# Kernel tuning notes

Measured on AMD Instinct MI355X. Metric: run time of the kernel, lower is better.

Reference implementation:

```python
import jax, jax.numpy as jnp
import numpy as np

BETA = 0.1
NUM_LAYERS = 2  # GT layers inside each FastGTN


def densify(edge_index, edge_weight, num_nodes):
    # edge_index: [T, 2, E] int, edge_weight: [T, E] -> dense [T, N, N]
    T, _, E = edge_index.shape
    t_ids = jnp.broadcast_to(jnp.arange(T)[:, None], (T, E))
    dense = jnp.zeros((T, num_nodes, num_nodes), dtype=edge_weight.dtype)
    return dense.at[t_ids, edge_index[:, 0, :], edge_index[:, 1, :]].add(edge_weight)


def fast_gtn(dense_A, X, Ws, conv_w, lin_w, lin_b, num_nodes):
    # Ws: [C, w_in, w_out]; conv_w: [L, C, T]; lin_w: [C*w_out, w_out]
    H = jnp.einsum('nk,ckh->cnh', X, Ws)              # [C, N, w_out]
    X_ = jax.lax.stop_gradient(H)                      # clone().detach()
    for l in range(NUM_LAYERS):
        filt = jax.nn.softmax(conv_w[l], axis=1)       # [C, T]
        adj = jnp.einsum('ct,tij->cij', filt, dense_A) # [C, N, N]
        H = jnp.einsum('cij,cjh->cih', adj, H)         # graph conv per channel
    H_ = jax.nn.relu(BETA * X_ + (1.0 - BETA) * H)     # [C, N, w_out]
    H_ = jnp.transpose(H_, (1, 0, 2)).reshape(num_nodes, -1)  # [N, C*w_out]
    return jax.nn.relu(H_ @ lin_w + lin_b)             # [N, w_out]


def setup_inputs() -> dict:
    key = jax.random.key(0)
    ks = jax.random.split(key, 12)
    T, E, N = 4, 131072, 4096
    C, F_IN, H_OUT = 2, 128, 64
    edge_index = jax.random.randint(ks[0], (T, 2, E), 0, N, dtype=jnp.int64)
    edge_weight = jax.random.uniform(ks[1], (T, E), dtype=jnp.float32)
    X = jax.random.normal(ks[2], (N, F_IN), dtype=jnp.float32)
    def glorot(k, shape):
        fan_in, fan_out = shape[-2], shape[-1]
        s = jnp.sqrt(6.0 / (fan_in + fan_out))
        return jax.random.uniform(k, shape, jnp.float32, -s, s)
    # FastGTN #1 (w_in=F_IN)
    Ws1 = glorot(ks[3], (C, F_IN, H_OUT))
    conv_w1 = 0.1 * jax.random.normal(ks[4], (NUM_LAYERS, C, T), dtype=jnp.float32)
    lin_w1 = glorot(ks[5], (C * H_OUT, H_OUT))
    lin_b1 = jnp.zeros((H_OUT,), jnp.float32)
    # FastGTN #2 (w_in=H_OUT)
    Ws2 = glorot(ks[6], (C, H_OUT, H_OUT))
    conv_w2 = 0.1 * jax.random.normal(ks[7], (NUM_LAYERS, C, T), dtype=jnp.float32)
    lin_w2 = glorot(ks[8], (C * H_OUT, H_OUT))
    lin_b2 = jnp.zeros((H_OUT,), jnp.float32)
    return {"edge_index": edge_index, "edge_weight": edge_weight, "X": X,
            "Ws1": Ws1, "conv_w1": conv_w1, "lin_w1": lin_w1, "lin_b1": lin_b1,
            "Ws2": Ws2, "conv_w2": conv_w2, "lin_w2": lin_w2, "lin_b2": lin_b2}


def reference(edge_index, edge_weight, X, Ws1, conv_w1, lin_w1, lin_b1,
              Ws2, conv_w2, lin_w2, lin_b2):
    N = X.shape[0]
    dense_A = densify(edge_index, edge_weight, N)      # [T, N, N]
    H = fast_gtn(dense_A, X, Ws1, conv_w1, lin_w1, lin_b1, N)
    H = fast_gtn(dense_A, H, Ws2, conv_w2, lin_w2, lin_b2, N)
    return H
```

## Files before the change

### kernel.cpp

```cpp
#include <hip/hip_runtime.h>

#define E_EDGES 131072
#define N_NODES 4096
#define HOUT    64
#define NE_TOT  (4 * E_EDGES)
#define CAP     256
#define CSTRIDE 16
#define SC_NBLK 64
#define SC_NTHR 1024
#define SC_EPB  (NE_TOT / SC_NBLK)
#define SC_EPT  (SC_EPB / SC_NTHR)

__device__ __forceinline__ unsigned short f2bf(float x) {
    unsigned u = __float_as_uint(x);
    return (unsigned short)((u + 0x7FFFu + ((u >> 16) & 1u)) >> 16);
}
__device__ __forceinline__ float bf2f(unsigned b) {
    return __uint_as_float(b << 16);
}

__device__ __forceinline__ void softmax4(const float* __restrict__ cw,
                                         int layer, int c, float f[4]) {
#pragma unroll
    for (int t = 0; t < 4; ++t) f[t] = cw[(layer * 2 + c) * 4 + t];
    float m = fmaxf(fmaxf(f[0], f[1]), fmaxf(f[2], f[3]));
    float s = 0.f;
#pragma unroll
    for (int t = 0; t < 4; ++t) { f[t] = expf(f[t] - m); s += f[t]; }
    float inv = 1.0f / s;
#pragma unroll
    for (int t = 0; t < 4; ++t) f[t] *= inv;
}

__device__ __forceinline__ float selw(const float f[4], int t) {
    float a = (t & 1) ? f[1] : f[0];
    float b = (t & 1) ? f[3] : f[2];
    return (t & 2) ? b : a;
}

__device__ __forceinline__ void fma8(float acc[8], float w, uint4 v) {
    acc[0] += w * bf2f(v.x & 0xFFFFu); acc[1] += w * bf2f(v.x >> 16);
    acc[2] += w * bf2f(v.y & 0xFFFFu); acc[3] += w * bf2f(v.y >> 16);
    acc[4] += w * bf2f(v.z & 0xFFFFu); acc[5] += w * bf2f(v.z >> 16);
    acc[6] += w * bf2f(v.w & 0xFFFFu); acc[7] += w * bf2f(v.w >> 16);
}

__device__ __forceinline__ uint4 pack8(const float acc[8]) {
    uint4 r;
    r.x = (unsigned)f2bf(acc[0]) | ((unsigned)f2bf(acc[1]) << 16);
    r.y = (unsigned)f2bf(acc[2]) | ((unsigned)f2bf(acc[3]) << 16);
    r.z = (unsigned)f2bf(acc[4]) | ((unsigned)f2bf(acc[5]) << 16);
    r.w = (unsigned)f2bf(acc[6]) | ((unsigned)f2bf(acc[7]) << 16);
    return r;
}

__device__ __forceinline__ void spmm_row2c(const unsigned* __restrict__ rowe, int len,
                                           const unsigned* __restrict__ H16,
                                           const float f0[4], const float f1[4],
                                           int lane, float a0[8], float a1[8]) {
    int g  = lane >> 3;
    int hq = lane & 7;
#pragma unroll
    for (int j = 0; j < 8; ++j) { a0[j] = 0.f; a1[j] = 0.f; }
    int e = 0;
    for (; e + 32 <= len; e += 32) {
        unsigned r0 = rowe[e + g];
        unsigned r1 = rowe[e + 8 + g];
        unsigned r2 = rowe[e + 16 + g];
        unsigned r3 = rowe[e + 24 + g];
        int   d0 = r0 & 0xFFF, t0 = (r0 >> 12) & 3;
        int   d1 = r1 & 0xFFF, t1 = (r1 >> 12) & 3;
        int   d2 = r2 & 0xFFF, t2 = (r2 >> 12) & 3;
        int   d3 = r3 & 0xFFF, t3 = (r3 >> 12) & 3;
        float w0 = bf2f(r0 >> 16), w1 = bf2f(r1 >> 16);
        float w2 = bf2f(r2 >> 16), w3 = bf2f(r3 >> 16);
        uint4 v00 = ((const uint4*)(H16 + (d0 * 2 + 0) * 32))[hq];
        uint4 v01 = ((const uint4*)(H16 + (d0 * 2 + 1) * 32))[hq];
        uint4 v10 = ((const uint4*)(H16 + (d1 * 2 + 0) * 32))[hq];
        uint4 v11 = ((const uint4*)(H16 + (d1 * 2 + 1) * 32))[hq];
        uint4 v20 = ((const uint4*)(H16 + (d2 * 2 + 0) * 32))[hq];
        uint4 v21 = ((const uint4*)(H16 + (d2 * 2 + 1) * 32))[hq];
        uint4 v30 = ((const uint4*)(H16 + (d3 * 2 + 0) * 32))[hq];
        uint4 v31 = ((const uint4*)(H16 + (d3 * 2 + 1) * 32))[hq];
        fma8(a0, w0 * selw(f0, t0), v00);
        fma8(a1, w0 * selw(f1, t0), v01);
        fma8(a0, w1 * selw(f0, t1), v10);
        fma8(a1, w1 * selw(f1, t1), v11);
        fma8(a0, w2 * selw(f0, t2), v20);
        fma8(a1, w2 * selw(f1, t2), v21);
        fma8(a0, w3 * selw(f0, t3), v30);
        fma8(a1, w3 * selw(f1, t3), v31);
    }
    for (; e + 8 <= len; e += 8) {
        unsigned r0 = rowe[e + g];
        int   d0 = r0 & 0xFFF, t0 = (r0 >> 12) & 3;
        float w0 = bf2f(r0 >> 16);
        uint4 v00 = ((const uint4*)(H16 + (d0 * 2 + 0) * 32))[hq];
        uint4 v01 = ((const uint4*)(H16 + (d0 * 2 + 1) * 32))[hq];
        fma8(a0, w0 * selw(f0, t0), v00);
        fma8(a1, w0 * selw(f1, t0), v01);
    }
    if (g < len - e) {
        unsigned r0 = rowe[e + g];
        int   d0 = r0 & 0xFFF, t0 = (r0 >> 12) & 3;
        float w0 = bf2f(r0 >> 16);
        uint4 v00 = ((const uint4*)(H16 + (d0 * 2 + 0) * 32))[hq];
        uint4 v01 = ((const uint4*)(H16 + (d0 * 2 + 1) * 32))[hq];
        fma8(a0, w0 * selw(f0, t0), v00);
        fma8(a1, w0 * selw(f1, t0), v01);
    }
#pragma unroll
    for (int j = 0; j < 8; ++j) {
        a0[j] += __shfl_xor(a0[j], 8);
        a0[j] += __shfl_xor(a0[j], 16);
        a0[j] += __shfl_xor(a0[j], 32);
        a1[j] += __shfl_xor(a1[j], 8);
        a1[j] += __shfl_xor(a1[j], 16);
        a1[j] += __shfl_xor(a1[j], 32);
    }
}

__global__ void __launch_bounds__(256)
zinit_kernel(const float* __restrict__ X, const float* __restrict__ Ws,
             float* __restrict__ H0, unsigned* __restrict__ H016,
             int* __restrict__ cursor) {
    int idx = blockIdx.x * 256 + threadIdx.x;
    if (idx < N_NODES * CSTRIDE) cursor[idx] = 0;
    int h = idx & 63;
    int n = (idx >> 6) & (N_NODES - 1);
    int c = idx >> 18;
    const float4* xv = (const float4*)(X + n * 128);
    const float*  w  = Ws + c * 128 * HOUT + h;
    float acc = 0.f;
#pragma unroll 8
    for (int k4 = 0; k4 < 32; ++k4) {
        float4 xx = xv[k4];
        acc += xx.x * w[(k4 * 4 + 0) * HOUT];
        acc += xx.y * w[(k4 * 4 + 1) * HOUT];
        acc += xx.z * w[(k4 * 4 + 2) * HOUT];
        acc += xx.w * w[(k4 * 4 + 3) * HOUT];
    }
    H0[idx] = acc;
    ((unsigned short*)H016)[(n * 2 + c) * HOUT + h] = f2bf(acc);
}

__global__ void __launch_bounds__(SC_NTHR)
scatter_kernel(const int* __restrict__ ei, const float* __restrict__ ew,
               int* __restrict__ gcursor, unsigned* __restrict__ edges) {
    __shared__ int shist[N_NODES];
    __shared__ int sbase[N_NODES];
    int tid = threadIdx.x;
    int t   = blockIdx.x >> 4;
    int e0  = (blockIdx.x & 15) * SC_EPB + tid * SC_EPT;
    const int*   ps = ei + (t * 2 + 0) * E_EDGES + e0;
    const int*   pd = ei + (t * 2 + 1) * E_EDGES + e0;
    const float* pw = ew + t * E_EDGES + e0;
#pragma unroll
    for (int j = 0; j < 4; ++j) shist[tid * 4 + j] = 0;
    __syncthreads();

    int4   s0 = ((const int4*)ps)[0],  s1 = ((const int4*)ps)[1];
    int4   d0 = ((const int4*)pd)[0],  d1 = ((const int4*)pd)[1];
    float4 w0 = ((const float4*)pw)[0], w1 = ((const float4*)pw)[1];
    int   srcs[8] = {s0.x, s0.y, s0.z, s0.w, s1.x, s1.y, s1.z, s1.w};
    int   dsts[8] = {d0.x, d0.y, d0.z, d0.w, d1.x, d1.y, d1.z, d1.w};
    float wts[8]  = {w0.x, w0.y, w0.z, w0.w, w1.x, w1.y, w1.z, w1.w};
    int lpos[8];
#pragma unroll
    for (int j = 0; j < 8; ++j) lpos[j] = atomicAdd(&shist[srcs[j]], 1);
    __syncthreads();

#pragma unroll
    for (int j = 0; j < 4; ++j) {
        int b = tid * 4 + j;
        int cntb = shist[b];
        if (cntb) sbase[b] = atomicAdd(&gcursor[b * CSTRIDE], cntb);
    }
    __syncthreads();

    unsigned tb = (unsigned)t << 12;
#pragma unroll
    for (int j = 0; j < 8; ++j) {
        unsigned p = (unsigned)(sbase[srcs[j]] + lpos[j]);
        unsigned rec = ((unsigned)f2bf(wts[j]) << 16) | tb | (unsigned)dsts[j];
        if (p < CAP) edges[srcs[j] * CAP + p] = rec;
    }
}

__global__ void __launch_bounds__(256)
spmm_kernel(const int* __restrict__ cnt, const unsigned* __restrict__ edges,
            const unsigned* __restrict__ Hin16, unsigned* __restrict__ Hout16,
            const float* __restrict__ cw) {
    int row  = (blockIdx.x * 256 + threadIdx.x) >> 6;
    int lane = threadIdx.x & 63;
    float f0[4], f1[4];
    softmax4(cw, 0, 0, f0);
    softmax4(cw, 0, 1, f1);
    int len = min(cnt[row * CSTRIDE], CAP);
    float a0[8], a1[8];
    spmm_row2c(edges + row * CAP, len, Hin16, f0, f1, lane, a0, a1);
    if ((lane >> 3) == 0) {
        int hq = lane & 7;
        ((uint4*)(Hout16 + (row * 2 + 0) * 32))[hq] = pack8(a0);
        ((uint4*)(Hout16 + (row * 2 + 1) * 32))[hq] = pack8(a1);
    }
}

template <bool FINAL>
__global__ void __launch_bounds__(256)
tail_kernel(const int* __restrict__ cnt, const unsigned* __restrict__ edges,
            const unsigned* __restrict__ Hin16,
            const float* __restrict__ H0,
            const float* __restrict__ cw,
            const float* __restrict__ lw, const float* __restrict__ lb,
            const float* __restrict__ Wsn,
            float* __restrict__ outp, unsigned* __restrict__ out16) {
    __shared__ float hcomb[4][2 * HOUT];
    __shared__ float mids[4][HOUT];
    int tid  = threadIdx.x;
    int r    = tid >> 6;
    int lane = tid & 63;
    int row  = blockIdx.x * 4 + r;

    float f0[4], f1[4];
    softmax4(cw, 1, 0, f0);
    softmax4(cw, 1, 1, f1);
    int len = min(cnt[row * CSTRIDE], CAP);
    float a0[8], a1[8];
    spmm_row2c(edges + row * CAP, len, Hin16, f0, f1, lane, a0, a1);

    if ((lane >> 3) == 0) {
        int hq = lane & 7;
#pragma unroll
        for (int j = 0; j < 8; ++j) {
            int h = hq * 8 + j;
            float h00 = H0[row * HOUT + h];
            float h01 = H0[(N_NODES + row) * HOUT + h];
            hcomb[r][h]        = fmaxf(0.1f * h00 + 0.9f * a0[j], 0.f);
            hcomb[r][HOUT + h] = fmaxf(0.1f * h01 + 0.9f * a1[j], 0.f);
        }
    }
    __syncthreads();

    float a = lb[lane];
#pragma unroll 8
    for (int j = 0; j < 2 * HOUT; ++j) a += hcomb[r][j] * lw[j * HOUT + lane];

    if (FINAL) {
        outp[row * HOUT + lane] = fmaxf(a, 0.f);
    } else {
        mids[r][lane] = fmaxf(a, 0.f);
        __syncthreads();
#pragma unroll
        for (int c = 0; c < 2; ++c) {
            float acc = 0.f;
            const float* w = Wsn + c * HOUT * HOUT + lane;
#pragma unroll 8
            for (int k = 0; k < HOUT; ++k) acc += mids[r][k] * w[k * HOUT];
            outp[(c * N_NODES + row) * HOUT + lane] = acc;
            ((unsigned short*)out16)[(row * 2 + c) * HOUT + lane] = f2bf(acc);
        }
    }
}

extern "C" void kernel_launch(void* const* d_in, const int* in_sizes, int n_in,
                              void* d_out, int out_size, void* d_ws, size_t ws_size,
                              hipStream_t stream) {
    const int*   ei  = (const int*)d_in[0];
    const float* ew  = (const float*)d_in[1];
    const float* X   = (const float*)d_in[2];
    const float* Ws1 = (const float*)d_in[3];
    const float* cw1 = (const float*)d_in[4];
    const float* lw1 = (const float*)d_in[5];
    const float* lb1 = (const float*)d_in[6];
    const float* Ws2 = (const float*)d_in[7];
    const float* cw2 = (const float*)d_in[8];
    const float* lw2 = (const float*)d_in[9];
    const float* lb2 = (const float*)d_in[10];
    float* outp = (float*)d_out;

    char* ws = (char*)d_ws;
    size_t off = 0;
    auto alloc = [&](size_t bytes) -> void* {
        void* p = ws + off;
        off += (bytes + 255) & ~size_t(255);
        return p;
    };
    int*      cursor = (int*)alloc((size_t)N_NODES * CSTRIDE * 4);
    unsigned* edges  = (unsigned*)alloc((size_t)N_NODES * CAP * 4);
    float*    H0a    = (float*)alloc((size_t)2 * N_NODES * HOUT * 4);
    unsigned* H0a16  = (unsigned*)alloc((size_t)2 * N_NODES * HOUT * 2);
    unsigned* Ha16   = (unsigned*)alloc((size_t)2 * N_NODES * HOUT * 2);
    float*    H0b    = (float*)alloc((size_t)2 * N_NODES * HOUT * 4);
    unsigned* H0b16  = (unsigned*)alloc((size_t)2 * N_NODES * HOUT * 2);

    zinit_kernel  <<<2048, 256, 0, stream>>>(X, Ws1, H0a, H0a16, cursor);
    scatter_kernel<<<SC_NBLK, SC_NTHR, 0, stream>>>(ei, ew, cursor, edges);

    spmm_kernel<<<1024, 256, 0, stream>>>(cursor, edges, H0a16, Ha16, cw1);
    tail_kernel<false><<<1024, 256, 0, stream>>>(
        cursor, edges, Ha16, H0a, cw1, lw1, lb1, Ws2, H0b, H0b16);

    spmm_kernel<<<1024, 256, 0, stream>>>(cursor, edges, H0b16, Ha16, cw2);
    tail_kernel<true><<<1024, 256, 0, stream>>>(
        cursor, edges, Ha16, H0b, cw2, lw2, lb2, nullptr, outp, nullptr);
}
```

Before: 102.1 us.

## Split each sparse row across two wavefronts with shared-memory partial reduction

Each row's edge list is now split between two wavefronts that take alternating 16-edge chunks, instead of one wavefront covering the whole row with a 32-edge unroll. The partial sums are combined through shared memory, and grids double to 2048 blocks of two rows each. In the non-final tail kernel, the two channels of the follow-up Ws projection go to the two wavefronts. The aim is more parallelism and more memory-level parallelism for the latency-bound gathers, at the cost of an extra barrier, shared-memory traffic and a smaller unroll per wave. The launch bounds also gain a minimum-blocks hint of 8.

Measured after the change: 103.6 us. About the same (+1.5%).

```diff
diff --git a/kernel.cpp b/kernel.cpp
--- a/kernel.cpp
+++ b/kernel.cpp
@@ -54,60 +54,52 @@
     return r;
 }
 
-__device__ __forceinline__ void spmm_row2c(const unsigned* __restrict__ rowe, int len,
-                                           const unsigned* __restrict__ H16,
-                                           const float f0[4], const float f1[4],
-                                           int lane, float a0[8], float a1[8]) {
+__device__ __forceinline__ void spmm_half(const unsigned* __restrict__ rowe, int len,
+                                          const unsigned* __restrict__ H16,
+                                          const float f0[4], const float f1[4],
+                                          int lane, int w, float a0[8], float a1[8]) {
     int g  = lane >> 3;
     int hq = lane & 7;
 #pragma unroll
     for (int j = 0; j < 8; ++j) { a0[j] = 0.f; a1[j] = 0.f; }
-    int e = 0;
-    for (; e + 32 <= len; e += 32) {
-        unsigned r0 = rowe[e + g];
-        unsigned r1 = rowe[e + 8 + g];
-        unsigned r2 = rowe[e + 16 + g];
-        unsigned r3 = rowe[e + 24 + g];
+    int nb = len >> 4;
+    for (int b = w; b < nb; b += 2) {
+        const unsigned* be = rowe + b * 16;
+        unsigned r0 = be[g];
+        unsigned r1 = be[8 + g];
         int   d0 = r0 & 0xFFF, t0 = (r0 >> 12) & 3;
         int   d1 = r1 & 0xFFF, t1 = (r1 >> 12) & 3;
-        int   d2 = r2 & 0xFFF, t2 = (r2 >> 12) & 3;
-        int   d3 = r3 & 0xFFF, t3 = (r3 >> 12) & 3;
         float w0 = bf2f(r0 >> 16), w1 = bf2f(r1 >> 16);
-        float w2 = bf2f(r2 >> 16), w3 = bf2f(r3 >> 16);
         uint4 v00 = ((const uint4*)(H16 + (d0 * 2 + 0) * 32))[hq];
         uint4 v01 = ((const uint4*)(H16 + (d0 * 2 + 1) * 32))[hq];
         uint4 v10 = ((const uint4*)(H16 + (d1 * 2 + 0) * 32))[hq];
         uint4 v11 = ((const uint4*)(H16 + (d1 * 2 + 1) * 32))[hq];
-        uint4 v20 = ((const uint4*)(H16 + (d2 * 2 + 0) * 32))[hq];
-        uint4 v21 = ((const uint4*)(H16 + (d2 * 2 + 1) * 32))[hq];
-        uint4 v30 = ((const uint4*)(H16 + (d3 * 2 + 0) * 32))[hq];
-        uint4 v31 = ((const uint4*)(H16 + (d3 * 2 + 1) * 32))[hq];
         fma8(a0, w0 * selw(f0, t0), v00);
         fma8(a1, w0 * selw(f1, t0), v01);
         fma8(a0, w1 * selw(f0, t1), v10);
         fma8(a1, w1 * selw(f1, t1), v11);
-        fma8(a0, w2 * selw(f0, t2), v20);
-        fma8(a1, w2 * selw(f1, t2), v21);
-        fma8(a0, w3 * selw(f0, t3), v30);
-        fma8(a1, w3 * selw(f1, t3), v31);
-    }
-    for (; e + 8 <= len; e += 8) {
-        unsigned r0 = rowe[e + g];
-        int   d0 = r0 & 0xFFF, t0 = (r0 >> 12) & 3;
-        float w0 = bf2f(r0 >> 16);
-        uint4 v00 = ((const uint4*)(H16 + (d0 * 2 + 0) * 32))[hq];
-        uint4 v01 = ((const uint4*)(H16 + (d0 * 2 + 1) * 32))[hq];
-        fma8(a0, w0 * selw(f0, t0), v00);
-        fma8(a1, w0 * selw(f1, t0), v01);
-    }
-    if (g < len - e) {
-        unsigned r0 = rowe[e + g];
-        int   d0 = r0 & 0xFFF, t0 = (r0 >> 12) & 3;
-        float w0 = bf2f(r0 >> 16);
-        uint4 v00 = ((const uint4*)(H16 + (d0 * 2 + 0) * 32))[hq];
-        uint4 v01 = ((const uint4*)(H16 + (d0 * 2 + 1) * 32))[hq];
-        fma8(a0, w0 * selw(f0, t0), v00);
-        fma8(a1, w0 * selw(f1, t0), v01);
+    }
+    int e = nb << 4;
+    if (e < len && (nb & 1) == w) {
+        if (e + 8 <= len) {
+            unsigned r0 = rowe[e + g];
+            int   d0 = r0 & 0xFFF, t0 = (r0 >> 12) & 3;
+            float w0 = bf2f(r0 >> 16);
+            uint4 v00 = ((const uint4*)(H16 + (d0 * 2 + 0) * 32))[hq];
+            uint4 v01 = ((const uint4*)(H16 + (d0 * 2 + 1) * 32))[hq];
+            fma8(a0, w0 * selw(f0, t0), v00);
+            fma8(a1, w0 * selw(f1, t0), v01);
+            e += 8;
+        }
+        if (g < len - e) {
+            unsigned r0 = rowe[e + g];
+            int   d0 = r0 & 0xFFF, t0 = (r0 >> 12) & 3;
+            float w0 = bf2f(r0 >> 16);
+            uint4 v00 = ((const uint4*)(H16 + (d0 * 2 + 0) * 32))[hq];
+            uint4 v01 = ((const uint4*)(H16 + (d0 * 2 + 1) * 32))[hq];
+            fma8(a0, w0 * selw(f0, t0), v00);
+            fma8(a1, w0 * selw(f1, t0), v01);
+        }
     }
 #pragma unroll
     for (int j = 0; j < 8; ++j) {
@@ -187,27 +179,46 @@
     }
 }
 
-__global__ void __launch_bounds__(256)
+__global__ void __launch_bounds__(256, 8)
 spmm_kernel(const int* __restrict__ cnt, const unsigned* __restrict__ edges,
             const unsigned* __restrict__ Hin16, unsigned* __restrict__ Hout16,
             const float* __restrict__ cw) {
-    int row  = (blockIdx.x * 256 + threadIdx.x) >> 6;
-    int lane = threadIdx.x & 63;
+    __shared__ float part[2][2][64];
+    int tid  = threadIdx.x;
+    int wid  = tid >> 6;
+    int lane = tid & 63;
+    int r    = wid >> 1;
+    int w    = wid & 1;
+    int row  = blockIdx.x * 2 + r;
     float f0[4], f1[4];
     softmax4(cw, 0, 0, f0);
     softmax4(cw, 0, 1, f1);
     int len = min(cnt[row * CSTRIDE], CAP);
     float a0[8], a1[8];
-    spmm_row2c(edges + row * CAP, len, Hin16, f0, f1, lane, a0, a1);
-    if ((lane >> 3) == 0) {
+    spmm_half(edges + row * CAP, len, Hin16, f0, f1, lane, w, a0, a1);
+    if (w == 1 && (lane >> 3) == 0) {
         int hq = lane & 7;
+#pragma unroll
+        for (int j = 0; j < 8; ++j) {
+            part[r][0][hq * 8 + j] = a0[j];
+            part[r][1][hq * 8 + j] = a1[j];
+        }
+    }
+    __syncthreads();
+    if (w == 0 && (lane >> 3) == 0) {
+        int hq = lane & 7;
+#pragma unroll
+        for (int j = 0; j < 8; ++j) {
+            a0[j] += part[r][0][hq * 8 + j];
+            a1[j] += part[r][1][hq * 8 + j];
+        }
         ((uint4*)(Hout16 + (row * 2 + 0) * 32))[hq] = pack8(a0);
         ((uint4*)(Hout16 + (row * 2 + 1) * 32))[hq] = pack8(a1);
     }
 }
 
 template <bool FINAL>
-__global__ void __launch_bounds__(256)
+__global__ void __launch_bounds__(256, 8)
 tail_kernel(const int* __restrict__ cnt, const unsigned* __restrict__ edges,
             const unsigned* __restrict__ Hin16,
             const float* __restrict__ H0,
@@ -215,50 +226,68 @@
             const float* __restrict__ lw, const float* __restrict__ lb,
             const float* __restrict__ Wsn,
             float* __restrict__ outp, unsigned* __restrict__ out16) {
-    __shared__ float hcomb[4][2 * HOUT];
-    __shared__ float mids[4][HOUT];
+    __shared__ float part[2][2][64];
+    __shared__ float hcomb[2][2 * HOUT];
+    __shared__ float mids[2][HOUT];
     int tid  = threadIdx.x;
-    int r    = tid >> 6;
+    int wid  = tid >> 6;
     int lane = tid & 63;
-    int row  = blockIdx.x * 4 + r;
+    int r    = wid >> 1;
+    int w    = wid & 1;
+    int row  = blockIdx.x * 2 + r;
 
     float f0[4], f1[4];
     softmax4(cw, 1, 0, f0);
     softmax4(cw, 1, 1, f1);
     int len = min(cnt[row * CSTRIDE], CAP);
     float a0[8], a1[8];
-    spmm_row2c(edges + row * CAP, len, Hin16, f0, f1, lane, a0, a1);
-
-    if ((lane >> 3) == 0) {
+    spmm_half(edges + row * CAP, len, Hin16, f0, f1, lane, w, a0, a1);
+    if (w == 1 && (lane >> 3) == 0) {
+        int hq = lane & 7;
+#pragma unroll
+        for (int j = 0; j < 8; ++j) {
+            part[r][0][hq * 8 + j] = a0[j];
+            part[r][1][hq * 8 + j] = a1[j];
+        }
+    }
+    __syncthreads();
+    if (w == 0 && (lane >> 3) == 0) {
         int hq = lane & 7;
 #pragma unroll
         for (int j = 0; j < 8; ++j) {
             int h = hq * 8 + j;
+            float s0 = a0[j] + part[r][0][hq * 8 + j];
+            float s1 = a1[j] + part[r][1][hq * 8 + j];
             float h00 = H0[row * HOUT + h];
             float h01 = H0[(N_NODES + row) * HOUT + h];
-            hcomb[r][h]        = fmaxf(0.1f * h00 + 0.9f * a0[j], 0.f);
-            hcomb[r][HOUT + h] = fmaxf(0.1f * h01 + 0.9f * a1[j], 0.f);
-        }
-    }
-    __syncthreads();
-
-    float a = lb[lane];
+            hcomb[r][h]        = fmaxf(0.1f * h00 + 0.9f * s0, 0.f);
+            hcomb[r][HOUT + h] = fmaxf(0.1f * h01 + 0.9f * s1, 0.f);
+        }
+    }
+    __syncthreads();
+
+    if (FINAL) {
+        if (w == 0) {
+            float a = lb[lane];
 #pragma unroll 8
-    for (int j = 0; j < 2 * HOUT; ++j) a += hcomb[r][j] * lw[j * HOUT + lane];
-
-    if (FINAL) {
-        outp[row * HOUT + lane] = fmaxf(a, 0.f);
+            for (int j = 0; j < 2 * HOUT; ++j) a += hcomb[r][j] * lw[j * HOUT + lane];
+            outp[row * HOUT + lane] = fmaxf(a, 0.f);
+        }
     } else {
-        mids[r][lane] = fmaxf(a, 0.f);
+        if (w == 0) {
+            float a = lb[lane];
+#pragma unroll 8
+            for (int j = 0; j < 2 * HOUT; ++j) a += hcomb[r][j] * lw[j * HOUT + lane];
+            mids[r][lane] = fmaxf(a, 0.f);
+        }
         __syncthreads();
-#pragma unroll
-        for (int c = 0; c < 2; ++c) {
+        {
             float acc = 0.f;
-            const float* w = Wsn + c * HOUT * HOUT + lane;
+            const float* wv = Wsn + w * HOUT * HOUT + lane;
 #pragma unroll 8
-            for (int k = 0; k < HOUT; ++k) acc += mids[r][k] * w[k * HOUT];
-            outp[(c * N_NODES + row) * HOUT + lane] = acc;
-            ((unsigned short*)out16)[(row * 2 + c) * HOUT + lane] = f2bf(acc);
+            for (int k = 0; k < HOUT; ++k) acc += mids[r][k] * wv[k * HOUT];
+            outp[(w * N_NODES + row) * HOUT + lane] = acc;
+            ((unsigned short*)out16)[(row * 2 + w) * HOUT + lane] = f2bf(acc);
         }
     }
 }
@@ -297,11 +326,11 @@
     zinit_kernel  <<<2048, 256, 0, stream>>>(X, Ws1, H0a, H0a16, cursor);
     scatter_kernel<<<SC_NBLK, SC_NTHR, 0, stream>>>(ei, ew, cursor, edges);
 
-    spmm_kernel<<<1024, 256, 0, stream>>>(cursor, edges, H0a16, Ha16, cw1);
-    tail_kernel<false><<<1024, 256, 0, stream>>>(
+    spmm_kernel<<<2048, 256, 0, stream>>>(cursor, edges, H0a16, Ha16, cw1);
+    tail_kernel<false><<<2048, 256, 0, stream>>>(
         cursor, edges, Ha16, H0a, cw1, lw1, lb1, Ws2, H0b, H0b16);
 
-    spmm_kernel<<<1024, 256, 0, stream>>>(cursor, edges, H0b16, Ha16, cw2);
-    tail_kernel<true><<<1024, 256, 0, stream>>>(
+    spmm_kernel<<<2048, 256, 0, stream>>>(cursor, edges, H0b16, Ha16, cw2);
+    tail_kernel<true><<<2048, 256, 0, stream>>>(
         cursor, edges, Ha16, H0b, cw2, lw2, lb2, nullptr, outp, nullptr);
 }
```
